# Kernel tuning notes

Hardware: AMD Instinct MI355X
Metric: run time of the kernel (lower is better)

## Reference

```python
import jax, jax.numpy as jnp
import numpy as np

BLOCK_SIZES = [256] * 8            # sum = N_CTX = 2048
B, H, D = 2, 16, 64
N_CTX = sum(BLOCK_SIZES)
SPARSITY_PATTERN = 'block_causal'  # row_starts = 0, row_ends = end of own block


def _build_masks(block_sizes, pattern):
    cs = np.cumsum([0] + list(block_sizes))
    row_ends = np.concatenate([np.full(bs, cs[i + 1], dtype=np.int32)
                               for i, bs in enumerate(block_sizes)])
    if pattern == 'block_diagonal':
        row_starts = np.concatenate([np.full(bs, cs[i], dtype=np.int32)
                                     for i, bs in enumerate(block_sizes)])
    elif pattern == 'block_causal':
        row_starts = np.zeros_like(row_ends)
    else:
        raise ValueError(pattern)
    return jnp.asarray(row_starts), jnp.asarray(row_ends)


def setup_inputs() -> dict:
    key = jax.random.key(0)
    kq, kk, kv = jax.random.split(key, 3)
    q = jax.random.normal(kq, (B, H, N_CTX, D), dtype=jnp.float32)
    k = jax.random.normal(kk, (B, H, N_CTX, D), dtype=jnp.float32)
    v = jax.random.normal(kv, (B, H, N_CTX, D), dtype=jnp.float32)
    row_starts, row_ends = _build_masks(BLOCK_SIZES, SPARSITY_PATTERN)
    sm_scale = jnp.float32(1.0 / np.sqrt(D))
    return {"q": q, "k": k, "v": v, "sm_scale": sm_scale,
            "row_starts": row_starts, "row_ends": row_ends}


def reference(q, k, v, sm_scale, row_starts, row_ends):
    # q,k,v: [B,H,N,D]; per query row i, attend to kv cols in [row_starts[i], row_ends[i])
    n = q.shape[2]
    cols = jnp.arange(n, dtype=jnp.int32)
    allowed = (cols[None, :] >= row_starts[:, None]) & (cols[None, :] < row_ends[:, None])  # [N,N]
    scores = jnp.einsum('bhqd,bhkd->bhqk', q, k) * sm_scale
    neg = jnp.finfo(scores.dtype).min
    scores = jnp.where(allowed[None, None], scores, neg)
    p = jax.nn.softmax(scores, axis=-1)
    return jnp.einsum('bhqk,bhkd->bhqd', p, v)
```

## Files before the change

kernel.cpp:

```cpp
#include <hip/hip_runtime.h>


typedef short bf16x8 __attribute__((ext_vector_type(8)));
typedef short bf16x4 __attribute__((ext_vector_type(4)));
typedef float f32x4  __attribute__((ext_vector_type(4)));

#define MFMA(A, B, C) __builtin_amdgcn_mfma_f32_16x16x32_bf16((A), (B), (C), 0, 0, 0)

__device__ __forceinline__ short f2bf(float f) {
    union { float f; unsigned u; } c; c.f = f;
    unsigned r = c.u + 0x7FFFu + ((c.u >> 16) & 1u);
    return (short)(r >> 16);
}

__global__ __launch_bounds__(512, 4)
void bsattn_kernel(const float* __restrict__ Q, const float* __restrict__ K,
                   const float* __restrict__ V, const float* __restrict__ SC,
                   const int* __restrict__ RS, const int* __restrict__ RE,
                   float* __restrict__ O)
{
    constexpr int N = 2048, D = 64, LSTR = 72;

    int wg   = blockIdx.x;
    int slot = wg >> 8;
    int r    = wg & 255;
    int i8   = r >> 5;
    int bh   = r & 31;
    int qt   = (slot == 0) ? (15 - i8) : i8;
    int q0   = qt << 7;

    int tid  = threadIdx.x;
    int wid  = tid >> 6;
    int lane = tid & 63;
    int n    = lane & 15;
    int g    = lane >> 4;

    const size_t bho = (size_t)bh * (N * D);
    const float* Qb = Q + bho;
    const float* Kb = K + bho;
    const float* Vb = V + bho;
    float*       Ob = O + bho;

    __shared__ __align__(16) short lk[64 * LSTR];
    __shared__ __align__(16) short lv[64 * LSTR];
    __shared__ int sb[2][4];

    if (tid < 128) {
        int rs = RS[q0 + tid];
        int re = RE[q0 + tid];
        int a = rs, b = rs, c = re, d = re;
        #pragma unroll
        for (int off = 32; off > 0; off >>= 1) {
            a = min(a, __shfl_xor(a, off));
            b = max(b, __shfl_xor(b, off));
            c = min(c, __shfl_xor(c, off));
            d = max(d, __shfl_xor(d, off));
        }
        if (lane == 0) { sb[wid][0] = a; sb[wid][1] = b; sb[wid][2] = c; sb[wid][3] = d; }
    }

    int myrow = q0 + wid * 16 + n;
    int rs_l  = RS[myrow];
    int re_l  = RE[myrow];

    float sscale = SC[0] * 1.44269504088896340736f;

    bf16x8 qf0, qf1;
    {
        const float* qp = Qb + (size_t)myrow * D + g * 8;
        float4 a0 = *(const float4*)(qp);
        float4 a1 = *(const float4*)(qp + 4);
        float4 b0 = *(const float4*)(qp + 32);
        float4 b1 = *(const float4*)(qp + 36);
        qf0[0] = f2bf(a0.x * sscale); qf0[1] = f2bf(a0.y * sscale);
        qf0[2] = f2bf(a0.z * sscale); qf0[3] = f2bf(a0.w * sscale);
        qf0[4] = f2bf(a1.x * sscale); qf0[5] = f2bf(a1.y * sscale);
        qf0[6] = f2bf(a1.z * sscale); qf0[7] = f2bf(a1.w * sscale);
        qf1[0] = f2bf(b0.x * sscale); qf1[1] = f2bf(b0.y * sscale);
        qf1[2] = f2bf(b0.z * sscale); qf1[3] = f2bf(b0.w * sscale);
        qf1[4] = f2bf(b1.x * sscale); qf1[5] = f2bf(b1.y * sscale);
        qf1[6] = f2bf(b1.z * sscale); qf1[7] = f2bf(b1.w * sscale);
    }

    __syncthreads();
    int rs_min = min(sb[0][0], sb[1][0]);
    int rs_max = max(sb[0][1], sb[1][1]);
    int re_min = min(sb[0][2], sb[1][2]);
    int re_max = max(sb[0][3], sb[1][3]);

    f32x4 acc0 = {0.f, 0.f, 0.f, 0.f};
    f32x4 acc1 = acc0, acc2 = acc0, acc3 = acc0;
    float m_run = -1e30f, l_run = 0.f;

    for (int kt = (rs_min & ~63); kt < re_max; kt += 64) {
        __syncthreads();
        #pragma unroll
        for (int it = 0; it < 2; ++it) {
            int f   = it * 512 + tid;
            int key = f >> 4;
            int d0  = (f & 15) << 2;
            float4 kv = *(const float4*)(Kb + (size_t)(kt + key) * D + d0);
            bf16x4 kp;
            kp[0] = f2bf(kv.x); kp[1] = f2bf(kv.y); kp[2] = f2bf(kv.z); kp[3] = f2bf(kv.w);
            *(bf16x4*)(&lk[key * LSTR + d0]) = kp;
            float4 vv = *(const float4*)(Vb + (size_t)(kt + key) * D + d0);
            lv[(d0 + 0) * LSTR + key] = f2bf(vv.x);
            lv[(d0 + 1) * LSTR + key] = f2bf(vv.y);
            lv[(d0 + 2) * LSTR + key] = f2bf(vv.z);
            lv[(d0 + 3) * LSTR + key] = f2bf(vv.w);
        }
        __syncthreads();

        #pragma unroll
        for (int half = 0; half < 2; ++half) {
            int kb0 = kt + half * 32;
            int row0 = half * 32 + ((n >> 2) << 3) + (n & 3);
            const bf16x8* a00 = (const bf16x8*)&lk[row0 * LSTR + g * 8];
            const bf16x8* a01 = (const bf16x8*)&lk[row0 * LSTR + 32 + g * 8];
            const bf16x8* a10 = (const bf16x8*)&lk[(row0 + 4) * LSTR + g * 8];
            const bf16x8* a11 = (const bf16x8*)&lk[(row0 + 4) * LSTR + 32 + g * 8];
            f32x4 s0 = {0.f, 0.f, 0.f, 0.f};
            f32x4 s1 = {0.f, 0.f, 0.f, 0.f};
            s0 = MFMA(*a00, qf0, s0);
            s0 = MFMA(*a01, qf1, s0);
            s1 = MFMA(*a10, qf0, s1);
            s1 = MFMA(*a11, qf1, s1);

            float sc8[8] = { s0[0], s0[1], s0[2], s0[3], s1[0], s1[1], s1[2], s1[3] };
            if (kb0 < rs_max || kb0 + 32 > re_min) {
                #pragma unroll
                for (int j = 0; j < 8; ++j) {
                    int key = kb0 + g * 8 + j;
                    if (key < rs_l || key >= re_l) sc8[j] = -1e30f;
                }
            }
            float tmax = sc8[0];
            #pragma unroll
            for (int j = 1; j < 8; ++j) tmax = fmaxf(tmax, sc8[j]);
            tmax = fmaxf(tmax, __shfl_xor(tmax, 16));
            tmax = fmaxf(tmax, __shfl_xor(tmax, 32));
            float m_new = fmaxf(m_run, tmax);
            float alpha = __builtin_amdgcn_exp2f(m_run - m_new);
            float psum = 0.f;
            bf16x8 pf;
            #pragma unroll
            for (int j = 0; j < 8; ++j) {
                float p = (sc8[j] > -0.5e30f) ? __builtin_amdgcn_exp2f(sc8[j] - m_new) : 0.f;
                psum += p;
                pf[j] = f2bf(p);
            }
            psum += __shfl_xor(psum, 16);
            psum += __shfl_xor(psum, 32);
            l_run = l_run * alpha + psum;
            m_run = m_new;

            int rbase = g << 2;
            float al0 = __shfl(alpha, rbase + 0);
            float al1 = __shfl(alpha, rbase + 1);
            float al2 = __shfl(alpha, rbase + 2);
            float al3 = __shfl(alpha, rbase + 3);
            acc0[0] *= al0; acc0[1] *= al1; acc0[2] *= al2; acc0[3] *= al3;
            acc1[0] *= al0; acc1[1] *= al1; acc1[2] *= al2; acc1[3] *= al3;
            acc2[0] *= al0; acc2[1] *= al1; acc2[2] *= al2; acc2[3] *= al3;
            acc3[0] *= al0; acc3[1] *= al1; acc3[2] *= al2; acc3[3] *= al3;

            int klocal = half * 32 + g * 8;
            const bf16x8* v0 = (const bf16x8*)&lv[(0  + n) * LSTR + klocal];
            const bf16x8* v1 = (const bf16x8*)&lv[(16 + n) * LSTR + klocal];
            const bf16x8* v2 = (const bf16x8*)&lv[(32 + n) * LSTR + klocal];
            const bf16x8* v3 = (const bf16x8*)&lv[(48 + n) * LSTR + klocal];
            acc0 = MFMA(pf, *v0, acc0);
            acc1 = MFMA(pf, *v1, acc1);
            acc2 = MFMA(pf, *v2, acc2);
            acc3 = MFMA(pf, *v3, acc3);
        }
    }

    float linv = 1.0f / l_run;
    int rbase = g << 2;
    float li[4];
    li[0] = __shfl(linv, rbase + 0);
    li[1] = __shfl(linv, rbase + 1);
    li[2] = __shfl(linv, rbase + 2);
    li[3] = __shfl(linv, rbase + 3);
    int orow = q0 + wid * 16 + rbase;
    #pragma unroll
    for (int reg = 0; reg < 4; ++reg) {
        float* rp = Ob + (size_t)(orow + reg) * D + n;
        rp[0]  = acc0[reg] * li[reg];
        rp[16] = acc1[reg] * li[reg];
        rp[32] = acc2[reg] * li[reg];
        rp[48] = acc3[reg] * li[reg];
    }
}

extern "C" void kernel_launch(void* const* d_in, const int* in_sizes, int n_in,
                              void* d_out, int out_size, void* d_ws, size_t ws_size,
                              hipStream_t stream) {
    const float* q  = (const float*)d_in[0];
    const float* k  = (const float*)d_in[1];
    const float* v  = (const float*)d_in[2];
    const float* sc = (const float*)d_in[3];
    const int* rs   = (const int*)d_in[4];
    const int* re   = (const int*)d_in[5];
    float* out      = (float*)d_out;
    bsattn_kernel<<<dim3(512), dim3(512), 0, stream>>>(q, k, v, sc, rs, re, out);
}
```

Baseline: 155.5 us.

## Pre-convert K/V to bf16 with transposed V and pair query tiles per block

Adds a pre-pass kernel that converts K to bf16 and V to a transposed bf16 layout in workspace, so the attention loop loads ready bf16 tiles with vector copies instead of converting fp32 per tile in every block. The main kernel now uses 256-thread blocks that each process two 64-row query tiles (one early and one late) sharing each K/V tile load, which balances causal work. It also switches the P conversion to a cheaper rounding and adds an XOR swizzle on the K rows in LDS. The cost is an extra kernel launch plus a full pass over K and V, and it falls back to in-loop conversion when the workspace is too small.

```diff
diff --git a/kernel.cpp b/kernel.cpp
--- a/kernel.cpp
+++ b/kernel.cpp
@@ -2,195 +2,298 @@
 
 
 typedef short bf16x8 __attribute__((ext_vector_type(8)));
-typedef short bf16x4 __attribute__((ext_vector_type(4)));
 typedef float f32x4  __attribute__((ext_vector_type(4)));
+typedef unsigned short u16;
+typedef u16 u16x8 __attribute__((ext_vector_type(8)));
 
 #define MFMA(A, B, C) __builtin_amdgcn_mfma_f32_16x16x32_bf16((A), (B), (C), 0, 0, 0)
 
-__device__ __forceinline__ short f2bf(float f) {
+__device__ __forceinline__ u16 f2bf_rne(float f) {
     union { float f; unsigned u; } c; c.f = f;
     unsigned r = c.u + 0x7FFFu + ((c.u >> 16) & 1u);
-    return (short)(r >> 16);
-}
-
-__global__ __launch_bounds__(512, 4)
-void bsattn_kernel(const float* __restrict__ Q, const float* __restrict__ K,
-                   const float* __restrict__ V, const float* __restrict__ SC,
-                   const int* __restrict__ RS, const int* __restrict__ RE,
-                   float* __restrict__ O)
+    return (u16)(r >> 16);
+}
+__device__ __forceinline__ u16 f2bf_fast(float f) {
+    union { float f; unsigned u; } c; c.f = f;
+    return (u16)((c.u + 0x8000u) >> 16);
+}
+
+__global__ __launch_bounds__(256)
+void preconv_kernel(const float* __restrict__ K, const float* __restrict__ V,
+                    u16* __restrict__ Kb, u16* __restrict__ Vt)
+{
+    constexpr int N = 2048, D = 64, LP = 80;
+    int bh = blockIdx.x >> 5;
+    int k0 = (blockIdx.x & 31) << 6;
+    int tid = threadIdx.x;
+    __shared__ __align__(16) u16 lt[64 * LP];
+    const size_t base = ((size_t)bh * N + k0) * D;
+    #pragma unroll
+    for (int c = 0; c < 2; ++c) {
+        int f = c * 256 + tid;
+        int key = f >> 3, d8 = (f & 7) << 3;
+        const float* kp = K + base + key * D + d8;
+        float4 x0 = *(const float4*)kp, x1 = *(const float4*)(kp + 4);
+        u16x8 kk;
+        kk[0] = f2bf_rne(x0.x); kk[1] = f2bf_rne(x0.y);
+        kk[2] = f2bf_rne(x0.z); kk[3] = f2bf_rne(x0.w);
+        kk[4] = f2bf_rne(x1.x); kk[5] = f2bf_rne(x1.y);
+        kk[6] = f2bf_rne(x1.z); kk[7] = f2bf_rne(x1.w);
+        *(u16x8*)&Kb[base + key * D + d8] = kk;
+        const float* vp = V + base + key * D + d8;
+        float4 y0 = *(const float4*)vp, y1 = *(const float4*)(vp + 4);
+        float yy[8] = { y0.x, y0.y, y0.z, y0.w, y1.x, y1.y, y1.z, y1.w };
+        #pragma unroll
+        for (int j = 0; j < 8; ++j) {
+            int d = d8 + j;
+            int kph = key ^ (((d >> 3) & 7) << 3);
+            lt[d * LP + kph] = f2bf_rne(yy[j]);
+        }
+    }
+    __syncthreads();
+    const size_t tb = (size_t)bh * D * N + k0;
+    #pragma unroll
+    for (int c = 0; c < 2; ++c) {
+        int f = c * 256 + tid;
+        int d = f >> 3, k8 = (f & 7) << 3;
+        int kph = k8 ^ (((d >> 3) & 7) << 3);
+        *(u16x8*)&Vt[tb + (size_t)d * N + k8] = *(const u16x8*)&lt[d * LP + kph];
+    }
+}
+
+template<bool PRE>
+__global__ __launch_bounds__(256, 2)
+void bsattn_main(const float* __restrict__ Q, const float* __restrict__ K,
+                 const float* __restrict__ V, const float* __restrict__ SC,
+                 const int* __restrict__ RS, const int* __restrict__ RE,
+                 float* __restrict__ O, const u16* __restrict__ Kb,
+                 const u16* __restrict__ Vt)
 {
     constexpr int N = 2048, D = 64, LSTR = 72;
-
-    int wg   = blockIdx.x;
-    int slot = wg >> 8;
-    int r    = wg & 255;
-    int i8   = r >> 5;
-    int bh   = r & 31;
-    int qt   = (slot == 0) ? (15 - i8) : i8;
-    int q0   = qt << 7;
-
-    int tid  = threadIdx.x;
-    int wid  = tid >> 6;
-    int lane = tid & 63;
-    int n    = lane & 15;
-    int g    = lane >> 4;
-
-    const size_t bho = (size_t)bh * (N * D);
-    const float* Qb = Q + bho;
-    const float* Kb = K + bho;
-    const float* Vb = V + bho;
-    float*       Ob = O + bho;
-
-    __shared__ __align__(16) short lk[64 * LSTR];
-    __shared__ __align__(16) short lv[64 * LSTR];
-    __shared__ int sb[2][4];
-
-    if (tid < 128) {
-        int rs = RS[q0 + tid];
-        int re = RE[q0 + tid];
-        int a = rs, b = rs, c = re, d = re;
-        #pragma unroll
-        for (int off = 32; off > 0; off >>= 1) {
-            a = min(a, __shfl_xor(a, off));
-            b = max(b, __shfl_xor(b, off));
-            c = min(c, __shfl_xor(c, off));
-            d = max(d, __shfl_xor(d, off));
-        }
-        if (lane == 0) { sb[wid][0] = a; sb[wid][1] = b; sb[wid][2] = c; sb[wid][3] = d; }
-    }
-
-    int myrow = q0 + wid * 16 + n;
-    int rs_l  = RS[myrow];
-    int re_l  = RE[myrow];
+    int pr = blockIdx.x >> 5;
+    int bh = blockIdx.x & 31;
+    int qA = 31 - pr, qB = pr;
+    int q0A = qA << 6, q0B = qB << 6;
+
+    int tid = threadIdx.x, wid = tid >> 6, lane = tid & 63;
+    int n = lane & 15, g = lane >> 4;
+
+    const size_t bho = (size_t)bh * N * D;
+    __shared__ __align__(16) u16 lk[64 * LSTR];
+    __shared__ __align__(16) u16 lv[64 * LSTR];
+    __shared__ int sb[2][4][4];
+
+    int rowA = q0A + wid * 16 + n, rowB = q0B + wid * 16 + n;
+    int rsA = RS[rowA], reA = RE[rowA];
+    int rsB = RS[rowB], reB = RE[rowB];
+    {
+        int a = rsA, b = rsA, c = reA, d = reA;
+        int e = rsB, h = rsB, i = reB, j = reB;
+        #pragma unroll
+        for (int o = 1; o < 16; o <<= 1) {
+            a = min(a, __shfl_xor(a, o)); b = max(b, __shfl_xor(b, o));
+            c = min(c, __shfl_xor(c, o)); d = max(d, __shfl_xor(d, o));
+            e = min(e, __shfl_xor(e, o)); h = max(h, __shfl_xor(h, o));
+            i = min(i, __shfl_xor(i, o)); j = max(j, __shfl_xor(j, o));
+        }
+        if (lane == 0) {
+            sb[0][wid][0] = a; sb[0][wid][1] = b; sb[0][wid][2] = c; sb[0][wid][3] = d;
+            sb[1][wid][0] = e; sb[1][wid][1] = h; sb[1][wid][2] = i; sb[1][wid][3] = j;
+        }
+    }
 
     float sscale = SC[0] * 1.44269504088896340736f;
 
-    bf16x8 qf0, qf1;
-    {
-        const float* qp = Qb + (size_t)myrow * D + g * 8;
-        float4 a0 = *(const float4*)(qp);
-        float4 a1 = *(const float4*)(qp + 4);
-        float4 b0 = *(const float4*)(qp + 32);
-        float4 b1 = *(const float4*)(qp + 36);
-        qf0[0] = f2bf(a0.x * sscale); qf0[1] = f2bf(a0.y * sscale);
-        qf0[2] = f2bf(a0.z * sscale); qf0[3] = f2bf(a0.w * sscale);
-        qf0[4] = f2bf(a1.x * sscale); qf0[5] = f2bf(a1.y * sscale);
-        qf0[6] = f2bf(a1.z * sscale); qf0[7] = f2bf(a1.w * sscale);
-        qf1[0] = f2bf(b0.x * sscale); qf1[1] = f2bf(b0.y * sscale);
-        qf1[2] = f2bf(b0.z * sscale); qf1[3] = f2bf(b0.w * sscale);
-        qf1[4] = f2bf(b1.x * sscale); qf1[5] = f2bf(b1.y * sscale);
-        qf1[6] = f2bf(b1.z * sscale); qf1[7] = f2bf(b1.w * sscale);
+    bf16x8 qA0, qA1, qB0, qB1;
+    {
+        const float* qp = Q + bho + (size_t)rowA * D + g * 8;
+        float4 a0 = *(const float4*)qp, a1 = *(const float4*)(qp + 4);
+        float4 b0 = *(const float4*)(qp + 32), b1 = *(const float4*)(qp + 36);
+        qA0[0] = f2bf_rne(a0.x * sscale); qA0[1] = f2bf_rne(a0.y * sscale);
+        qA0[2] = f2bf_rne(a0.z * sscale); qA0[3] = f2bf_rne(a0.w * sscale);
+        qA0[4] = f2bf_rne(a1.x * sscale); qA0[5] = f2bf_rne(a1.y * sscale);
+        qA0[6] = f2bf_rne(a1.z * sscale); qA0[7] = f2bf_rne(a1.w * sscale);
+        qA1[0] = f2bf_rne(b0.x * sscale); qA1[1] = f2bf_rne(b0.y * sscale);
+        qA1[2] = f2bf_rne(b0.z * sscale); qA1[3] = f2bf_rne(b0.w * sscale);
+        qA1[4] = f2bf_rne(b1.x * sscale); qA1[5] = f2bf_rne(b1.y * sscale);
+        qA1[6] = f2bf_rne(b1.z * sscale); qA1[7] = f2bf_rne(b1.w * sscale);
+    }
+    {
+        const float* qp = Q + bho + (size_t)rowB * D + g * 8;
+        float4 a0 = *(const float4*)qp, a1 = *(const float4*)(qp + 4);
+        float4 b0 = *(const float4*)(qp + 32), b1 = *(const float4*)(qp + 36);
+        qB0[0] = f2bf_rne(a0.x * sscale); qB0[1] = f2bf_rne(a0.y * sscale);
+        qB0[2] = f2bf_rne(a0.z * sscale); qB0[3] = f2bf_rne(a0.w * sscale);
+        qB0[4] = f2bf_rne(a1.x * sscale); qB0[5] = f2bf_rne(a1.y * sscale);
+        qB0[6] = f2bf_rne(a1.z * sscale); qB0[7] = f2bf_rne(a1.w * sscale);
+        qB1[0] = f2bf_rne(b0.x * sscale); qB1[1] = f2bf_rne(b0.y * sscale);
+        qB1[2] = f2bf_rne(b0.z * sscale); qB1[3] = f2bf_rne(b0.w * sscale);
+        qB1[4] = f2bf_rne(b1.x * sscale); qB1[5] = f2bf_rne(b1.y * sscale);
+        qB1[6] = f2bf_rne(b1.z * sscale); qB1[7] = f2bf_rne(b1.w * sscale);
     }
 
     __syncthreads();
-    int rs_min = min(sb[0][0], sb[1][0]);
-    int rs_max = max(sb[0][1], sb[1][1]);
-    int re_min = min(sb[0][2], sb[1][2]);
-    int re_max = max(sb[0][3], sb[1][3]);
-
-    f32x4 acc0 = {0.f, 0.f, 0.f, 0.f};
-    f32x4 acc1 = acc0, acc2 = acc0, acc3 = acc0;
-    float m_run = -1e30f, l_run = 0.f;
-
-    for (int kt = (rs_min & ~63); kt < re_max; kt += 64) {
-        __syncthreads();
-        #pragma unroll
-        for (int it = 0; it < 2; ++it) {
-            int f   = it * 512 + tid;
-            int key = f >> 4;
-            int d0  = (f & 15) << 2;
-            float4 kv = *(const float4*)(Kb + (size_t)(kt + key) * D + d0);
-            bf16x4 kp;
-            kp[0] = f2bf(kv.x); kp[1] = f2bf(kv.y); kp[2] = f2bf(kv.z); kp[3] = f2bf(kv.w);
-            *(bf16x4*)(&lk[key * LSTR + d0]) = kp;
-            float4 vv = *(const float4*)(Vb + (size_t)(kt + key) * D + d0);
-            lv[(d0 + 0) * LSTR + key] = f2bf(vv.x);
-            lv[(d0 + 1) * LSTR + key] = f2bf(vv.y);
-            lv[(d0 + 2) * LSTR + key] = f2bf(vv.z);
-            lv[(d0 + 3) * LSTR + key] = f2bf(vv.w);
-        }
-        __syncthreads();
-
-        #pragma unroll
-        for (int half = 0; half < 2; ++half) {
-            int kb0 = kt + half * 32;
-            int row0 = half * 32 + ((n >> 2) << 3) + (n & 3);
-            const bf16x8* a00 = (const bf16x8*)&lk[row0 * LSTR + g * 8];
-            const bf16x8* a01 = (const bf16x8*)&lk[row0 * LSTR + 32 + g * 8];
-            const bf16x8* a10 = (const bf16x8*)&lk[(row0 + 4) * LSTR + g * 8];
-            const bf16x8* a11 = (const bf16x8*)&lk[(row0 + 4) * LSTR + 32 + g * 8];
-            f32x4 s0 = {0.f, 0.f, 0.f, 0.f};
-            f32x4 s1 = {0.f, 0.f, 0.f, 0.f};
-            s0 = MFMA(*a00, qf0, s0);
-            s0 = MFMA(*a01, qf1, s0);
-            s1 = MFMA(*a10, qf0, s1);
-            s1 = MFMA(*a11, qf1, s1);
-
-            float sc8[8] = { s0[0], s0[1], s0[2], s0[3], s1[0], s1[1], s1[2], s1[3] };
-            if (kb0 < rs_max || kb0 + 32 > re_min) {
+    int mnA = min(min(sb[0][0][0], sb[0][1][0]), min(sb[0][2][0], sb[0][3][0]));
+    int mxA = max(max(sb[0][0][1], sb[0][1][1]), max(sb[0][2][1], sb[0][3][1]));
+    int nmA = min(min(sb[0][0][2], sb[0][1][2]), min(sb[0][2][2], sb[0][3][2]));
+    int xA  = max(max(sb[0][0][3], sb[0][1][3]), max(sb[0][2][3], sb[0][3][3]));
+    int mnB = min(min(sb[1][0][0], sb[1][1][0]), min(sb[1][2][0], sb[1][3][0]));
+    int mxB = max(max(sb[1][0][1], sb[1][1][1]), max(sb[1][2][1], sb[1][3][1]));
+    int nmB = min(min(sb[1][0][2], sb[1][1][2]), min(sb[1][2][2], sb[1][3][2]));
+    int xB  = max(max(sb[1][0][3], sb[1][1][3]), max(sb[1][2][3], sb[1][3][3]));
+
+    f32x4 aA[4], aB[4];
+    #pragma unroll
+    for (int c = 0; c < 4; ++c) { aA[c] = (f32x4){0.f,0.f,0.f,0.f}; aB[c] = aA[c]; }
+    float mA = -1e30f, lA = 0.f, mB = -1e30f, lB = 0.f;
+
+    const int base0 = ((n >> 2) << 3) + (n & 3) + (((n >> 2) & 1) << 2);
+
+    auto process = [&](const bf16x8& qf0, const bf16x8& qf1, f32x4* acc,
+                       float& m_run, float& l_run, int rs_l, int re_l,
+                       int rs_mx, int re_mn, int kt) {
+        float sc[16];
+        #pragma unroll
+        for (int h = 0; h < 2; ++h) {
+            int r0 = h * 32 + base0;
+            const u16* p0 = &lk[r0 * LSTR + g * 8];
+            const u16* p1 = &lk[(r0 ^ 4) * LSTR + g * 8];
+            f32x4 t0 = {0.f,0.f,0.f,0.f}, t1 = t0;
+            t0 = MFMA(*(const bf16x8*)p0,        qf0, t0);
+            t0 = MFMA(*(const bf16x8*)(p0 + 32), qf1, t0);
+            t1 = MFMA(*(const bf16x8*)p1,        qf0, t1);
+            t1 = MFMA(*(const bf16x8*)(p1 + 32), qf1, t1);
+            #pragma unroll
+            for (int r = 0; r < 4; ++r) { sc[h*8 + r] = t0[r]; sc[h*8 + 4 + r] = t1[r]; }
+        }
+        if (kt < rs_mx || kt + 64 > re_mn) {
+            #pragma unroll
+            for (int h = 0; h < 2; ++h)
                 #pragma unroll
                 for (int j = 0; j < 8; ++j) {
-                    int key = kb0 + g * 8 + j;
-                    if (key < rs_l || key >= re_l) sc8[j] = -1e30f;
+                    int key = kt + h * 32 + g * 8 + j;
+                    if (key < rs_l || key >= re_l) sc[h*8 + j] = -1e30f;
                 }
+        }
+        float tmax = sc[0];
+        #pragma unroll
+        for (int j = 1; j < 16; ++j) tmax = fmaxf(tmax, sc[j]);
+        tmax = fmaxf(tmax, __shfl_xor(tmax, 16));
+        tmax = fmaxf(tmax, __shfl_xor(tmax, 32));
+        float m_new = fmaxf(m_run, tmax);
+        float alpha = __builtin_amdgcn_exp2f(m_run - m_new);
+        float ps = 0.f;
+        bf16x8 pf0, pf1;
+        #pragma unroll
+        for (int j = 0; j < 8; ++j) {
+            float p = __builtin_amdgcn_exp2f(sc[j] - m_new);
+            ps += p; pf0[j] = (short)f2bf_fast(p);
+        }
+        #pragma unroll
+        for (int j = 0; j < 8; ++j) {
+            float p = __builtin_amdgcn_exp2f(sc[8 + j] - m_new);
+            ps += p; pf1[j] = (short)f2bf_fast(p);
+        }
+        ps += __shfl_xor(ps, 16);
+        ps += __shfl_xor(ps, 32);
+        l_run = l_run * alpha + ps;
+        m_run = m_new;
+        int rb = g << 2;
+        float a0 = __shfl(alpha, rb + 0), a1 = __shfl(alpha, rb + 1);
+        float a2 = __shfl(alpha, rb + 2), a3 = __shfl(alpha, rb + 3);
+        #pragma unroll
+        for (int c = 0; c < 4; ++c) {
+            acc[c][0] *= a0; acc[c][1] *= a1; acc[c][2] *= a2; acc[c][3] *= a3;
+        }
+        #pragma unroll
+        for (int h = 0; h < 2; ++h) {
+            int kl = h * 32 + g * 8;
+            const bf16x8& pf = h ? pf1 : pf0;
+            acc[0] = MFMA(pf, *(const bf16x8*)&lv[(0  + n) * LSTR + kl], acc[0]);
+            acc[1] = MFMA(pf, *(const bf16x8*)&lv[(16 + n) * LSTR + kl], acc[1]);
+            acc[2] = MFMA(pf, *(const bf16x8*)&lv[(32 + n) * LSTR + kl], acc[2]);
+            acc[3] = MFMA(pf, *(const bf16x8*)&lv[(48 + n) * LSTR + kl], acc[3]);
+        }
+    };
+
+    int kstart = min(mnA, mnB) & ~63;
+    int kend   = max(xA, xB);
+    for (int kt = kstart; kt < kend; kt += 64) {
+        __syncthreads();
+        if (PRE) {
+            const u16* __restrict__ KbB = Kb + bho + (size_t)kt * D;
+            const u16* __restrict__ VtB = Vt + (size_t)bh * D * N + kt;
+            #pragma unroll
+            for (int c = 0; c < 2; ++c) {
+                int f = c * 256 + tid;
+                int a0i = f >> 3;
+                int b8  = (f & 7) << 3;
+                int kp  = a0i ^ (((a0i >> 3) & 1) << 2);
+                *(u16x8*)&lk[kp  * LSTR + b8] = *(const u16x8*)&KbB[a0i * D + b8];
+                *(u16x8*)&lv[a0i * LSTR + b8] = *(const u16x8*)&VtB[(size_t)a0i * N + b8];
             }
-            float tmax = sc8[0];
+        } else {
+            const float* KB = K + bho + (size_t)kt * D;
+            const float* VB = V + bho + (size_t)kt * D;
             #pragma unroll
-            for (int j = 1; j < 8; ++j) tmax = fmaxf(tmax, sc8[j]);
-            tmax = fmaxf(tmax, __shfl_xor(tmax, 16));
-            tmax = fmaxf(tmax, __shfl_xor(tmax, 32));
-            float m_new = fmaxf(m_run, tmax);
-            float alpha = __builtin_amdgcn_exp2f(m_run - m_new);
-            float psum = 0.f;
-            bf16x8 pf;
-            #pragma unroll
-            for (int j = 0; j < 8; ++j) {
-                float p = (sc8[j] > -0.5e30f) ? __builtin_amdgcn_exp2f(sc8[j] - m_new) : 0.f;
-                psum += p;
-                pf[j] = f2bf(p);
+            for (int c = 0; c < 2; ++c) {
+                int f = c * 256 + tid;
+                int key = f >> 3, d8 = (f & 7) << 3;
+                int kp = key ^ (((key >> 3) & 1) << 2);
+                const float* kq = KB + key * D + d8;
+                float4 x0 = *(const float4*)kq, x1 = *(const float4*)(kq + 4);
+                u16x8 kk;
+                kk[0] = f2bf_rne(x0.x); kk[1] = f2bf_rne(x0.y);
+                kk[2] = f2bf_rne(x0.z); kk[3] = f2bf_rne(x0.w);
+                kk[4] = f2bf_rne(x1.x); kk[5] = f2bf_rne(x1.y);
+                kk[6] = f2bf_rne(x1.z); kk[7] = f2bf_rne(x1.w);
+                *(u16x8*)&lk[kp * LSTR + d8] = kk;
+                const float* vq = VB + key * D + d8;
+                float4 y0 = *(const float4*)vq, y1 = *(const float4*)(vq + 4);
+                lv[(d8+0)*LSTR+key] = f2bf_rne(y0.x); lv[(d8+1)*LSTR+key] = f2bf_rne(y0.y);
+                lv[(d8+2)*LSTR+key] = f2bf_rne(y0.z); lv[(d8+3)*LSTR+key] = f2bf_rne(y0.w);
+                lv[(d8+4)*LSTR+key] = f2bf_rne(y1.x); lv[(d8+5)*LSTR+key] = f2bf_rne(y1.y);
+                lv[(d8+6)*LSTR+key] = f2bf_rne(y1.z); lv[(d8+7)*LSTR+key] = f2bf_rne(y1.w);
             }
-            psum += __shfl_xor(psum, 16);
-            psum += __shfl_xor(psum, 32);
-            l_run = l_run * alpha + psum;
-            m_run = m_new;
-
-            int rbase = g << 2;
-            float al0 = __shfl(alpha, rbase + 0);
-            float al1 = __shfl(alpha, rbase + 1);
-            float al2 = __shfl(alpha, rbase + 2);
-            float al3 = __shfl(alpha, rbase + 3);
-            acc0[0] *= al0; acc0[1] *= al1; acc0[2] *= al2; acc0[3] *= al3;
-            acc1[0] *= al0; acc1[1] *= al1; acc1[2] *= al2; acc1[3] *= al3;
-            acc2[0] *= al0; acc2[1] *= al1; acc2[2] *= al2; acc2[3] *= al3;
-            acc3[0] *= al0; acc3[1] *= al1; acc3[2] *= al2; acc3[3] *= al3;
-
-            int klocal = half * 32 + g * 8;
-            const bf16x8* v0 = (const bf16x8*)&lv[(0  + n) * LSTR + klocal];
-            const bf16x8* v1 = (const bf16x8*)&lv[(16 + n) * LSTR + klocal];
-            const bf16x8* v2 = (const bf16x8*)&lv[(32 + n) * LSTR + klocal];
-            const bf16x8* v3 = (const bf16x8*)&lv[(48 + n) * LSTR + klocal];
-            acc0 = MFMA(pf, *v0, acc0);
-            acc1 = MFMA(pf, *v1, acc1);
-            acc2 = MFMA(pf, *v2, acc2);
-            acc3 = MFMA(pf, *v3, acc3);
-        }
-    }
-
-    float linv = 1.0f / l_run;
-    int rbase = g << 2;
-    float li[4];
-    li[0] = __shfl(linv, rbase + 0);
-    li[1] = __shfl(linv, rbase + 1);
-    li[2] = __shfl(linv, rbase + 2);
-    li[3] = __shfl(linv, rbase + 3);
-    int orow = q0 + wid * 16 + rbase;
-    #pragma unroll
-    for (int reg = 0; reg < 4; ++reg) {
-        float* rp = Ob + (size_t)(orow + reg) * D + n;
-        rp[0]  = acc0[reg] * li[reg];
-        rp[16] = acc1[reg] * li[reg];
-        rp[32] = acc2[reg] * li[reg];
-        rp[48] = acc3[reg] * li[reg];
+        }
+        __syncthreads();
+        if (kt < xA && kt + 64 > mnA)
+            process(qA0, qA1, aA, mA, lA, rsA, reA, mxA, nmA, kt);
+        if (kt < xB && kt + 64 > mnB)
+            process(qB0, qB1, aB, mB, lB, rsB, reB, mxB, nmB, kt);
+    }
+
+    {
+        float linv = 1.0f / lA;
+        int rb = g << 2;
+        float l0 = __shfl(linv, rb + 0), l1 = __shfl(linv, rb + 1);
+        float l2 = __shfl(linv, rb + 2), l3 = __shfl(linv, rb + 3);
+        float li[4] = { l0, l1, l2, l3 };
+        int orow = q0A + wid * 16 + rb;
+        #pragma unroll
+        for (int r = 0; r < 4; ++r) {
+            float* rp = O + bho + (size_t)(orow + r) * D + n;
+            rp[0]  = aA[0][r] * li[r];
+            rp[16] = aA[1][r] * li[r];
+            rp[32] = aA[2][r] * li[r];
+            rp[48] = aA[3][r] * li[r];
+        }
+    }
+    {
+        float linv = 1.0f / lB;
+        int rb = g << 2;
+        float l0 = __shfl(linv, rb + 0), l1 = __shfl(linv, rb + 1);
+        float l2 = __shfl(linv, rb + 2), l3 = __shfl(linv, rb + 3);
+        float li[4] = { l0, l1, l2, l3 };
+        int orow = q0B + wid * 16 + rb;
+        #pragma unroll
+        for (int r = 0; r < 4; ++r) {
+            float* rp = O + bho + (size_t)(orow + r) * D + n;
+            rp[0]  = aB[0][r] * li[r];
+            rp[16] = aB[1][r] * li[r];
+            rp[32] = aB[2][r] * li[r];
+            rp[48] = aB[3][r] * li[r];
+        }
     }
 }
 
@@ -204,5 +307,17 @@
     const int* rs   = (const int*)d_in[4];
     const int* re   = (const int*)d_in[5];
     float* out      = (float*)d_out;
-    bsattn_kernel<<<dim3(512), dim3(512), 0, stream>>>(q, k, v, sc, rs, re, out);
-}
+
+    const size_t elems = 32ull * 2048 * 64;
+    const size_t need  = 2 * elems * sizeof(u16);
+    if (ws_size >= need) {
+        u16* Kb = (u16*)d_ws;
+        u16* Vt = Kb + elems;
+        preconv_kernel<<<dim3(1024), dim3(256), 0, stream>>>(k, v, Kb, Vt);
+        bsattn_main<true><<<dim3(512), dim3(256), 0, stream>>>(q, k, v, sc, rs, re, out, Kb, Vt);
+    } else {
+        bsattn_main<false><<<dim3(512), dim3(256), 0, stream>>>(q, k, v, sc, rs, re, out,
+                                                                (const u16*)nullptr,
+                                                                (const u16*)nullptr);
+    }
+}
```

Result: faster. 149.1 us (-4.1%).
